# Kernel optimization log

Hardware: AMD Instinct MI355X
Metric: run time of the kernel (lower is better)

## Reference

```python
import jax, jax.numpy as jnp
import numpy as np
import math

B, S, HID = 2, 2048, 2048
NH, NKV, HD = 16, 4, 128
N_REP = NH // NKV
THETA = 1000000.0


def apply_rope(x, position_ids, theta=THETA):
    # x: (B, H, S, D), position_ids: (B, S)
    d = x.shape[-1]
    freqs = 1.0 / (theta ** (jnp.arange(0, d, 2, dtype=jnp.float32) / d))  # (D/2,)
    angles = position_ids.astype(jnp.float32)[:, :, None] * freqs[None, None, :]  # (B,S,D/2)
    cos = jnp.cos(angles)[:, None, :, :]  # (B,1,S,D/2)
    sin = jnp.sin(angles)[:, None, :, :]
    x_even = x[..., 0::2]
    x_odd = x[..., 1::2]
    rot_even = x_even * cos - x_odd * sin
    rot_odd = x_even * sin + x_odd * cos
    out = jnp.stack([rot_even, rot_odd], axis=-1)  # (B,H,S,D/2,2)
    return out.reshape(x.shape)


def setup_inputs() -> dict:
    key = jax.random.key(0)
    ks = jax.random.split(key, 6)
    x = jax.random.normal(ks[0], (B, S, HID), dtype=jnp.float32)
    position_ids = jnp.broadcast_to(jnp.arange(S, dtype=jnp.int64)[None, :], (B, S))
    # causal additive mask: 0 on/below diagonal, large negative above
    causal = jnp.where(jnp.tril(jnp.ones((S, S), dtype=bool)), 0.0, -1e9).astype(jnp.float32)
    attention_mask = jnp.broadcast_to(causal[None, None, :, :], (B, 1, S, S))
    sc = 1.0 / math.sqrt(HID)
    Wq = jax.random.normal(ks[1], (HID, NH * HD), dtype=jnp.float32) * sc
    Wk = jax.random.normal(ks[2], (HID, NKV * HD), dtype=jnp.float32) * sc
    Wv = jax.random.normal(ks[3], (HID, NKV * HD), dtype=jnp.float32) * sc
    Wo = jax.random.normal(ks[4], (NH * HD, HID), dtype=jnp.float32) * sc
    return {"x": x, "position_ids": position_ids, "attention_mask": attention_mask,
            "Wq": Wq, "Wk": Wk, "Wv": Wv, "Wo": Wo}


def reference(x, position_ids, attention_mask, Wq, Wk, Wv, Wo):
    b, s, _ = x.shape
    q = (x @ Wq).reshape(b, s, NH, HD).transpose(0, 2, 1, 3)   # (B,NH,S,D)
    k = (x @ Wk).reshape(b, s, NKV, HD).transpose(0, 2, 1, 3)  # (B,NKV,S,D)
    v = (x @ Wv).reshape(b, s, NKV, HD).transpose(0, 2, 1, 3)
    q = apply_rope(q, position_ids)
    k = apply_rope(k, position_ids)
    # repeat_kv: expand KV heads to match Q heads
    k = jnp.repeat(k, N_REP, axis=1)  # (B,NH,S,D)
    v = jnp.repeat(v, N_REP, axis=1)
    scale = 1.0 / math.sqrt(HD)
    scores = jnp.einsum('bhqd,bhkd->bhqk', q, k) * scale
    scores = scores + attention_mask
    attn = jax.nn.softmax(scores, axis=-1)
    out = jnp.einsum('bhqk,bhkd->bhqd', attn, v)
    out = out.transpose(0, 2, 1, 3).reshape(b, s, NH * HD)
    return out @ Wo
```

## Files before the change

kernel.cpp:

```cpp
#include <hip/hip_runtime.h>
#include <hip/hip_bf16.h>

#define S_LEN 2048
#define HID_D 2048
#define NH 16
#define NKV 4
#define HD 128
#define BATCH 2

typedef __hip_bfloat16 bf16;
using f32x4 = __attribute__((ext_vector_type(4))) float;
using s16x8 = __attribute__((ext_vector_type(8))) short;

struct TrueT { static constexpr bool value = true; };
struct FalseT { static constexpr bool value = false; };

__device__ __forceinline__ f32x4 mfma_16x16x32(s16x8 a, s16x8 b, f32x4 c) {
  return __builtin_amdgcn_mfma_f32_16x16x32_bf16(a, b, c, 0, 0, 0);
}

__device__ __forceinline__ void gload16(const void* g, void* l) {
  __builtin_amdgcn_global_load_lds(
      (const __attribute__((address_space(1))) void*)g,
      (__attribute__((address_space(3))) void*)l, 16, 0, 0);
}

__device__ __forceinline__ unsigned int pk2bf(float a, float b) {
  __hip_bfloat16 lo = __float2bfloat16(a), hi = __float2bfloat16(b);
  return ((unsigned int)*(unsigned short*)&hi << 16) | *(unsigned short*)&lo;
}

__global__ __launch_bounds__(256) void convert_bf16_k(const float* __restrict__ in,
                                                      bf16* __restrict__ out) {
  int i = (blockIdx.x * 256 + threadIdx.x) * 4;
  float4 v = *(const float4*)&in[i];
  out[i + 0] = __float2bfloat16(v.x);
  out[i + 1] = __float2bfloat16(v.y);
  out[i + 2] = __float2bfloat16(v.z);
  out[i + 3] = __float2bfloat16(v.w);
}

__global__ __launch_bounds__(256) void transpose_convert_k(const float* __restrict__ in,
                                                           bf16* __restrict__ out,
                                                           int K, int N) {
  __shared__ float tile[32][33];
  int n0 = blockIdx.x * 32, k0 = blockIdx.y * 32;
  int tx = threadIdx.x, ty = threadIdx.y;
#pragma unroll
  for (int i = ty; i < 32; i += 8) tile[i][tx] = in[(size_t)(k0 + i) * N + n0 + tx];
  __syncthreads();
#pragma unroll
  for (int i = ty; i < 32; i += 8)
    out[(size_t)(n0 + i) * K + k0 + tx] = __float2bfloat16(tile[tx][i]);
}

__global__ __launch_bounds__(512) void gemm256_k(const bf16* __restrict__ A,
                                                 const bf16* __restrict__ Bt,
                                                 float* __restrict__ C,
                                                 int M, int N, int K) {
  __shared__ bf16 Asm[2][256 * 64];
  __shared__ bf16 Bsm[2][256 * 64];
  const int tid = threadIdx.x;
  const int lane = tid & 63, wid = tid >> 6;
  const int fr = lane & 15, hi = lane >> 4;

  const int bid = blockIdx.y * gridDim.x + blockIdx.x;
  const int nwg = gridDim.x * gridDim.y;
  const int swz = (bid & 7) * (nwg >> 3) + (bid >> 3);
  const int m0 = (swz % gridDim.x) * 256;
  const int n0 = (swz / gridDim.x) * 256;

  const bf16* Ag = A + (size_t)m0 * K;
  const bf16* Bg = Bt + (size_t)n0 * K;

  auto stageHalf = [&](const bf16* src, bf16* ldsBase, int hr0, int k0) {
#pragma unroll
    for (int c = 0; c < 2; ++c) {
      int byte = tid * 16 + c * 8192;
      int row = byte >> 7;
      int col = byte & 127;
      int colSw = col ^ ((row & 7) << 4);
      gload16((const char*)(src + (size_t)(hr0 + row) * K + k0) + colSw,
              (char*)ldsBase + hr0 * 128 + byte);
    }
  };

  f32x4 acc[4][4][2];
#pragma unroll
  for (int p = 0; p < 4; ++p)
#pragma unroll
    for (int m = 0; m < 4; ++m)
#pragma unroll
      for (int n = 0; n < 2; ++n) acc[p][m][n] = (f32x4){0.f, 0.f, 0.f, 0.f};

  const int NT = K >> 6;
  stageHalf(Ag, &Asm[0][0], 0, 0);
  stageHalf(Bg, &Bsm[0][0], 0, 0);
  stageHalf(Bg, &Bsm[0][0], 128, 0);
  stageHalf(Ag, &Asm[0][0], 128, 0);
  asm volatile("s_waitcnt vmcnt(4)" ::: "memory");
  __builtin_amdgcn_s_barrier();

  for (int t = 0; t < NT; ++t) {
    const int cur = t & 1;
    const int nxt = cur ^ 1;
    const int kn = (t + 1) << 6;
    const bool more = (t + 1) < NT;
#pragma unroll
    for (int p = 0; p < 4; ++p) {
      const int r0 = (p >> 1) * 128 + (wid >> 2) * 64;
      const int c0 = (p & 1) * 128 + (wid & 3) * 32;
      s16x8 af[2][4], bq[2][2];
#pragma unroll
      for (int ks = 0; ks < 2; ++ks) {
#pragma unroll
        for (int m = 0; m < 4; ++m) {
          int r = r0 + m * 16 + fr;
          int cb = (ks * 64 + hi * 16) ^ ((r & 7) << 4);
          af[ks][m] = *(const s16x8*)((const char*)&Asm[cur][0] + r * 128 + cb);
        }
#pragma unroll
        for (int n = 0; n < 2; ++n) {
          int bn = c0 + n * 16 + fr;
          int cb = (ks * 64 + hi * 16) ^ ((bn & 7) << 4);
          bq[ks][n] = *(const s16x8*)((const char*)&Bsm[cur][0] + bn * 128 + cb);
        }
      }
      if (more) {
        if (p == 0) stageHalf(Ag, &Asm[nxt][0], 0, kn);
        else if (p == 1) stageHalf(Bg, &Bsm[nxt][0], 0, kn);
        else if (p == 2) stageHalf(Bg, &Bsm[nxt][0], 128, kn);
        else stageHalf(Ag, &Asm[nxt][0], 128, kn);
        asm volatile("s_waitcnt vmcnt(4)" ::: "memory");
      } else {
        if (p == 0) asm volatile("s_waitcnt vmcnt(2)" ::: "memory");
        else if (p == 1) asm volatile("s_waitcnt vmcnt(0)" ::: "memory");
      }
      __builtin_amdgcn_s_barrier();

      __builtin_amdgcn_s_setprio(1);
#pragma unroll
      for (int m = 0; m < 4; ++m)
#pragma unroll
        for (int n = 0; n < 2; ++n) {
          acc[p][m][n] = mfma_16x16x32(af[0][m], bq[0][n], acc[p][m][n]);
          acc[p][m][n] = mfma_16x16x32(af[1][m], bq[1][n], acc[p][m][n]);
        }
      __builtin_amdgcn_s_setprio(0);
    }
  }

#pragma unroll
  for (int p = 0; p < 4; ++p) {
    const int r0 = (p >> 1) * 128 + (wid >> 2) * 64;
    const int c0 = (p & 1) * 128 + (wid & 3) * 32;
#pragma unroll
    for (int m = 0; m < 4; ++m)
#pragma unroll
      for (int n = 0; n < 2; ++n) {
        const int row = m0 + r0 + m * 16 + hi * 4;
        const int col = n0 + c0 + n * 16 + fr;
#pragma unroll
        for (int r = 0; r < 4; ++r)
          C[(size_t)(row + r) * N + col] = acc[p][m][n][r];
      }
  }
}

__global__ __launch_bounds__(512) void gemm128n_k(const bf16* __restrict__ A,
                                                  const bf16* __restrict__ Bt,
                                                  float* __restrict__ C,
                                                  int M, int N, int K) {
  __shared__ bf16 Asm[2][256 * 64];
  __shared__ bf16 Bsm[2][128 * 64];
  const int tid = threadIdx.x;
  const int lane = tid & 63, wid = tid >> 6;
  const int fr = lane & 15, hi = lane >> 4;

  const int bid = blockIdx.y * gridDim.x + blockIdx.x;
  const int nwg = gridDim.x * gridDim.y;
  const int swz = (bid & 7) * (nwg >> 3) + (bid >> 3);
  const int m0 = (swz % gridDim.x) * 256;
  const int n0 = (swz / gridDim.x) * 128;

  const bf16* Ag = A + (size_t)m0 * K;
  const bf16* Bg = Bt + (size_t)n0 * K;

  auto stageHalf = [&](const bf16* src, bf16* ldsBase, int hr0, int k0) {
#pragma unroll
    for (int c = 0; c < 2; ++c) {
      int byte = tid * 16 + c * 8192;
      int row = byte >> 7;
      int col = byte & 127;
      int colSw = col ^ ((row & 7) << 4);
      gload16((const char*)(src + (size_t)(hr0 + row) * K + k0) + colSw,
              (char*)ldsBase + hr0 * 128 + byte);
    }
  };

  f32x4 acc[2][4][2];
#pragma unroll
  for (int p = 0; p < 2; ++p)
#pragma unroll
    for (int m = 0; m < 4; ++m)
#pragma unroll
      for (int n = 0; n < 2; ++n) acc[p][m][n] = (f32x4){0.f, 0.f, 0.f, 0.f};

  const int NT = K >> 6;
  stageHalf(Bg, &Bsm[0][0], 0, 0);
  stageHalf(Ag, &Asm[0][0], 0, 0);
  stageHalf(Ag, &Asm[0][0], 128, 0);
  asm volatile("s_waitcnt vmcnt(2)" ::: "memory");
  __builtin_amdgcn_s_barrier();

  for (int t = 0; t < NT; ++t) {
    const int cur = t & 1;
    const int nxt = cur ^ 1;
    const int kn = (t + 1) << 6;
    const bool more = (t + 1) < NT;
#pragma unroll
    for (int p = 0; p < 2; ++p) {
      const int r0 = p * 128 + (wid >> 2) * 64;
      const int c0 = (wid & 3) * 32;
      s16x8 af[2][4], bq[2][2];
#pragma unroll
      for (int ks = 0; ks < 2; ++ks) {
#pragma unroll
        for (int m = 0; m < 4; ++m) {
          int r = r0 + m * 16 + fr;
          int cb = (ks * 64 + hi * 16) ^ ((r & 7) << 4);
          af[ks][m] = *(const s16x8*)((const char*)&Asm[cur][0] + r * 128 + cb);
        }
#pragma unroll
        for (int n = 0; n < 2; ++n) {
          int bn = c0 + n * 16 + fr;
          int cb = (ks * 64 + hi * 16) ^ ((bn & 7) << 4);
          bq[ks][n] = *(const s16x8*)((const char*)&Bsm[cur][0] + bn * 128 + cb);
        }
      }
      if (more) {
        if (p == 0) {
          stageHalf(Bg, &Bsm[nxt][0], 0, kn);
          stageHalf(Ag, &Asm[nxt][0], 0, kn);
        } else {
          stageHalf(Ag, &Asm[nxt][0], 128, kn);
        }
        asm volatile("s_waitcnt vmcnt(2)" ::: "memory");
      } else {
        if (p == 0) asm volatile("s_waitcnt vmcnt(0)" ::: "memory");
      }
      __builtin_amdgcn_s_barrier();

      __builtin_amdgcn_s_setprio(1);
#pragma unroll
      for (int m = 0; m < 4; ++m)
#pragma unroll
        for (int n = 0; n < 2; ++n) {
          acc[p][m][n] = mfma_16x16x32(af[0][m], bq[0][n], acc[p][m][n]);
          acc[p][m][n] = mfma_16x16x32(af[1][m], bq[1][n], acc[p][m][n]);
        }
      __builtin_amdgcn_s_setprio(0);
    }
  }

#pragma unroll
  for (int p = 0; p < 2; ++p) {
    const int r0 = p * 128 + (wid >> 2) * 64;
    const int c0 = (wid & 3) * 32;
#pragma unroll
    for (int m = 0; m < 4; ++m)
#pragma unroll
      for (int n = 0; n < 2; ++n) {
        const int row = m0 + r0 + m * 16 + hi * 4;
        const int col = n0 + c0 + n * 16 + fr;
#pragma unroll
        for (int r = 0; r < 4; ++r)
          C[(size_t)(row + r) * N + col] = acc[p][m][n][r];
      }
  }
}

__global__ __launch_bounds__(256) void rope_q_k(const float* __restrict__ qkv,
                                                const int* __restrict__ pos_ids,
                                                bf16* __restrict__ Q) {
  int idx = blockIdx.x * 256 + threadIdx.x;
  int i = idx & 63;
  int h = (idx >> 6) & 15;
  int s = (idx >> 10) & 2047;
  int b = idx >> 21;
  const float kscale = 0.12751841418861862f;
  float pos = (float)pos_ids[b * S_LEN + s];
  float freq = exp2f((float)i * -0.31143075889569023f);
  float ang = pos * freq;
  float sn, cs;
  sincosf(ang, &sn, &cs);
  const float* src = qkv + (size_t)(b * S_LEN + s) * 3072 + h * HD + 2 * i;
  float e = src[0], o = src[1];
  bf16* dst = Q + ((size_t)(b * NH + h) * S_LEN + s) * HD + 2 * i;
  dst[0] = __float2bfloat16((e * cs - o * sn) * kscale);
  dst[1] = __float2bfloat16((e * sn + o * cs) * kscale);
}

__global__ __launch_bounds__(256) void rope_k_k(const float* __restrict__ qkv,
                                                const int* __restrict__ pos_ids,
                                                bf16* __restrict__ Kd) {
  int idx = blockIdx.x * 256 + threadIdx.x;
  int i = idx & 63;
  int kvh = (idx >> 6) & 3;
  int s = (idx >> 8) & 2047;
  int b = idx >> 19;
  float pos = (float)pos_ids[b * S_LEN + s];
  float freq = exp2f((float)i * -0.31143075889569023f);
  float ang = pos * freq;
  float sn, cs;
  sincosf(ang, &sn, &cs);
  const float* src = qkv + (size_t)(b * S_LEN + s) * 3072 + 2048 + kvh * HD + 2 * i;
  float e = src[0], o = src[1];
  bf16* dst = Kd + ((size_t)(b * NKV + kvh) * S_LEN + s) * HD + 2 * i;
  dst[0] = __float2bfloat16(e * cs - o * sn);
  dst[1] = __float2bfloat16(e * sn + o * cs);
}

__global__ __launch_bounds__(256) void v_trans_k(const float* __restrict__ qkv,
                                                 bf16* __restrict__ Vt) {
  __shared__ float tile[32][33];
  const int tx = threadIdx.x, ty = threadIdx.y;
  const int s0 = blockIdx.x * 32;
  const int d0 = blockIdx.y * 32;
  const int b = blockIdx.z >> 2, kvh = blockIdx.z & 3;
  const float* src = qkv + 2560 + kvh * HD;
#pragma unroll
  for (int i = ty; i < 32; i += 8)
    tile[i][tx] = src[(size_t)(b * S_LEN + s0 + i) * 3072 + d0 + tx];
  __syncthreads();
  bf16* dst = Vt + (size_t)(b * NKV + kvh) * HD * S_LEN;
#pragma unroll
  for (int i = ty; i < 32; i += 8)
    dst[(size_t)(d0 + i) * S_LEN + s0 + tx] = __float2bfloat16(tile[tx][i]);
}

__global__ __launch_bounds__(256) void attn_k(const bf16* __restrict__ Q,
                                              const bf16* __restrict__ K,
                                              const bf16* __restrict__ Vt,
                                              bf16* __restrict__ Aout) {
  __shared__ bf16 Ks[2][64 * 128];
  __shared__ bf16 Vs[2][128 * 64];
  __shared__ bf16 Ps[4][16 * 64];

  const int lane = threadIdx.x & 63;
  const int wid = threadIdx.x >> 6;
  const int fr = lane & 15;
  const int hi = lane >> 4;
  const int pi = blockIdx.x, h = blockIdx.y, b = blockIdx.z;
  const int kvh = h >> 2;
  const bf16* Qh = Q + (size_t)(b * NH + h) * S_LEN * HD;
  const bf16* Kh = K + (size_t)(b * NKV + kvh) * S_LEN * HD;
  const bf16* Vh = Vt + (size_t)(b * NKV + kvh) * HD * S_LEN;

  const int oB = lane * 16;
  const int rinK = oB >> 8;
  const int rinV = oB >> 7;
  bf16* myP = &Ps[wid][0];
  const int pswz = (fr & 7) << 4;

  auto stageKV = [&](int bufi, int kv0) {
#pragma unroll
    for (int c = 0; c < 4; ++c) {
      int absr = wid * 16 + c * 4 + rinK;
      int colb = (oB & 255) ^ (((absr >> 2) & 7) << 4);
      gload16((const char*)Kh + (size_t)(kv0 + absr) * 256 + colb,
              (char*)&Ks[bufi][0] + (wid * 16 + c * 4) * 256);
    }
#pragma unroll
    for (int c = 0; c < 4; ++c) {
      int absd = wid * 32 + c * 8 + rinV;
      int colb = (oB & 127) ^ ((absd & 7) << 4);
      gload16((const char*)Vh + (size_t)absd * (S_LEN * 2) + (size_t)kv0 * 2 + colb,
              (char*)&Vs[bufi][0] + (wid * 32 + c * 8) * 128);
    }
  };

#pragma unroll 1
  for (int t = 0; t < 2; ++t) {
    const int qb = t ? (31 - pi) : pi;
    const int q0w = qb * 64 + wid * 16;
    const int nsteps = qb + 1;

    s16x8 qf[4];
#pragma unroll
    for (int ks = 0; ks < 4; ++ks)
      qf[ks] = *(const s16x8*)&Qh[(size_t)(q0w + fr) * HD + ks * 32 + hi * 8];

    f32x4 o[8];
#pragma unroll
    for (int ds = 0; ds < 8; ++ds) o[ds] = (f32x4){0.f, 0.f, 0.f, 0.f};
    float lacc[4];
#pragma unroll
    for (int r = 0; r < 4; ++r) lacc[r] = 0.f;

    auto doStep = [&](int kv0, int bufc, auto LASTC) {
      constexpr bool LAST = decltype(LASTC)::value;
      f32x4 sg[4];
#pragma unroll
      for (int kv = 0; kv < 4; ++kv) {
        f32x4 a = (f32x4){0.f, 0.f, 0.f, 0.f};
        const int row = 4 * fr + kv;
#pragma unroll
        for (int ks = 0; ks < 4; ++ks) {
          int cb = (ks * 64 + hi * 16) ^ (((row >> 2) & 7) << 4);
          s16x8 kf = *(const s16x8*)((const char*)&Ks[bufc][0] + row * 256 + cb);
          a = mfma_16x16x32(qf[ks], kf, a);
        }
        sg[kv] = a;
      }

#pragma unroll
      for (int r = 0; r < 4; ++r) {
        float p0 = __builtin_exp2f(sg[0][r]);
        float p1 = __builtin_exp2f(sg[1][r]);
        float p2 = __builtin_exp2f(sg[2][r]);
        float p3 = __builtin_exp2f(sg[3][r]);
        if (LAST) {
          const int qrow = q0w + hi * 4 + r;
          const int kb = kv0 + 4 * fr;
          p0 = (kb <= qrow) ? p0 : 0.f;
          p1 = (kb + 1 <= qrow) ? p1 : 0.f;
          p2 = (kb + 2 <= qrow) ? p2 : 0.f;
          p3 = (kb + 3 <= qrow) ? p3 : 0.f;
        }
        lacc[r] += (p0 + p1) + (p2 + p3);
        const int prow = hi * 4 + r;
        uint2 pv;
        pv.x = pk2bf(p0, p1);
        pv.y = pk2bf(p2, p3);
        *(uint2*)((char*)myP + prow * 128 + ((fr * 8) ^ ((prow & 7) << 4))) = pv;
      }
      __builtin_amdgcn_wave_barrier();

      s16x8 pf[2];
#pragma unroll
      for (int g = 0; g < 2; ++g) {
        int cb = (g * 64 + hi * 16) ^ pswz;
        pf[g] = *(const s16x8*)((const char*)myP + fr * 128 + cb);
      }
      __builtin_amdgcn_wave_barrier();
#pragma unroll
      for (int ds = 0; ds < 8; ++ds) {
#pragma unroll
        for (int g = 0; g < 2; ++g) {
          int d = ds * 16 + fr;
          int cb = (g * 64 + hi * 16) ^ ((d & 7) << 4);
          s16x8 vf = *(const s16x8*)((const char*)&Vs[bufc][0] + d * 128 + cb);
          o[ds] = mfma_16x16x32(pf[g], vf, o[ds]);
        }
      }
    };

    int buf = 0;
    stageKV(0, 0);
    __syncthreads();

    for (int s = 0; s < nsteps - 1; ++s) {
      stageKV(buf ^ 1, s * 64 + 64);
      doStep(s * 64, buf, FalseT{});
      __syncthreads();
      buf ^= 1;
    }
    doStep((nsteps - 1) * 64, buf, TrueT{});
    __syncthreads();

#pragma unroll
    for (int r = 0; r < 4; ++r) {
      float l = lacc[r];
      l += __shfl_xor(l, 1, 16);
      l += __shfl_xor(l, 2, 16);
      l += __shfl_xor(l, 4, 16);
      l += __shfl_xor(l, 8, 16);
      float inv = 1.0f / l;
      const int srow = q0w + hi * 4 + r;
      bf16* orow = Aout + ((size_t)b * S_LEN + srow) * HID_D + h * HD;
#pragma unroll
      for (int ds = 0; ds < 8; ++ds)
        orow[ds * 16 + fr] = __float2bfloat16(o[ds][r] * inv);
    }
  }
}

extern "C" void kernel_launch(void* const* d_in, const int* in_sizes, int n_in,
                              void* d_out, int out_size, void* d_ws, size_t ws_size,
                              hipStream_t stream) {
  const float* x = (const float*)d_in[0];
  const int* pos = (const int*)d_in[1];
  const float* Wq = (const float*)d_in[3];
  const float* Wk = (const float*)d_in[4];
  const float* Wv = (const float*)d_in[5];
  const float* Wo = (const float*)d_in[6];
  float* out = (float*)d_out;

  char* ws = (char*)d_ws;
  size_t off = 0;
  auto alloc = [&](size_t bytes) {
    char* p = ws + off;
    off += (bytes + 255) & ~(size_t)255;
    return p;
  };
  bf16* xb = (bf16*)alloc((size_t)4096 * 2048 * 2);
  bf16* WqkvT = (bf16*)alloc((size_t)3072 * 2048 * 2);
  bf16* WoT = (bf16*)alloc((size_t)2048 * 2048 * 2);
  float* qkv = (float*)alloc((size_t)4096 * 3072 * 4);
  bf16* Qb = (bf16*)alloc((size_t)BATCH * NH * S_LEN * HD * 2);
  bf16* Kb = (bf16*)alloc((size_t)BATCH * NKV * S_LEN * HD * 2);
  bf16* Vtb = (bf16*)alloc((size_t)BATCH * NKV * HD * S_LEN * 2);
  bf16* aout = (bf16*)qkv;

  convert_bf16_k<<<8192, 256, 0, stream>>>(x, xb);
  dim3 tb(32, 8);
  transpose_convert_k<<<dim3(64, 64), tb, 0, stream>>>(Wq, WqkvT, 2048, 2048);
  transpose_convert_k<<<dim3(16, 64), tb, 0, stream>>>(Wk, WqkvT + (size_t)2048 * 2048, 2048, 512);
  transpose_convert_k<<<dim3(16, 64), tb, 0, stream>>>(Wv, WqkvT + (size_t)2560 * 2048, 2048, 512);
  transpose_convert_k<<<dim3(64, 64), tb, 0, stream>>>(Wo, WoT, 2048, 2048);

  gemm256_k<<<dim3(16, 12), 512, 0, stream>>>(xb, WqkvT, qkv, 4096, 3072, 2048);

  rope_q_k<<<16384, 256, 0, stream>>>(qkv, pos, Qb);
  rope_k_k<<<4096, 256, 0, stream>>>(qkv, pos, Kb);
  v_trans_k<<<dim3(64, 4, 8), tb, 0, stream>>>(qkv, Vtb);

  attn_k<<<dim3(16, NH, BATCH), 256, 0, stream>>>(Qb, Kb, Vtb, aout);

  gemm128n_k<<<dim3(16, 16), 512, 0, stream>>>(aout, WoT, out, 4096, 2048, 2048);
}
```

Baseline: 218.4 us.

## Store QKV projection in bf16 and widen attention query tile to 128 rows

The QKV GEMM now writes bf16 instead of fp32. This halves the intermediate buffer traffic read by the rope and V-transpose kernels. The attention kernel now handles 32 query rows per wave (128 per block) with two accumulator sets, so each K/V fragment loaded from LDS feeds two MFMAs. The grid is halved, which doubles per-wave register use and reduces the number of blocks available for load balancing. The qkv intermediate also loses precision by being rounded to bf16 before the rope step.

```diff
diff --git a/kernel.cpp b/kernel.cpp
--- a/kernel.cpp
+++ b/kernel.cpp
@@ -11,9 +11,6 @@
 typedef __hip_bfloat16 bf16;
 using f32x4 = __attribute__((ext_vector_type(4))) float;
 using s16x8 = __attribute__((ext_vector_type(8))) short;
-
-struct TrueT { static constexpr bool value = true; };
-struct FalseT { static constexpr bool value = false; };
 
 __device__ __forceinline__ f32x4 mfma_16x16x32(s16x8 a, s16x8 b, f32x4 c) {
   return __builtin_amdgcn_mfma_f32_16x16x32_bf16(a, b, c, 0, 0, 0);
@@ -56,7 +53,7 @@
 
 __global__ __launch_bounds__(512) void gemm256_k(const bf16* __restrict__ A,
                                                  const bf16* __restrict__ Bt,
-                                                 float* __restrict__ C,
+                                                 bf16* __restrict__ C,
                                                  int M, int N, int K) {
   __shared__ bf16 Asm[2][256 * 64];
   __shared__ bf16 Bsm[2][256 * 64];
@@ -162,7 +159,7 @@
         const int col = n0 + c0 + n * 16 + fr;
 #pragma unroll
         for (int r = 0; r < 4; ++r)
-          C[(size_t)(row + r) * N + col] = acc[p][m][n][r];
+          C[(size_t)(row + r) * N + col] = __float2bfloat16(acc[p][m][n][r]);
       }
   }
 }
@@ -280,7 +277,7 @@
   }
 }
 
-__global__ __launch_bounds__(256) void rope_q_k(const float* __restrict__ qkv,
+__global__ __launch_bounds__(256) void rope_q_k(const bf16* __restrict__ qkv,
                                                 const int* __restrict__ pos_ids,
                                                 bf16* __restrict__ Q) {
   int idx = blockIdx.x * 256 + threadIdx.x;
@@ -294,14 +291,14 @@
   float ang = pos * freq;
   float sn, cs;
   sincosf(ang, &sn, &cs);
-  const float* src = qkv + (size_t)(b * S_LEN + s) * 3072 + h * HD + 2 * i;
-  float e = src[0], o = src[1];
+  const bf16* src = qkv + (size_t)(b * S_LEN + s) * 3072 + h * HD + 2 * i;
+  float e = __bfloat162float(src[0]), o = __bfloat162float(src[1]);
   bf16* dst = Q + ((size_t)(b * NH + h) * S_LEN + s) * HD + 2 * i;
   dst[0] = __float2bfloat16((e * cs - o * sn) * kscale);
   dst[1] = __float2bfloat16((e * sn + o * cs) * kscale);
 }
 
-__global__ __launch_bounds__(256) void rope_k_k(const float* __restrict__ qkv,
+__global__ __launch_bounds__(256) void rope_k_k(const bf16* __restrict__ qkv,
                                                 const int* __restrict__ pos_ids,
                                                 bf16* __restrict__ Kd) {
   int idx = blockIdx.x * 256 + threadIdx.x;
@@ -314,29 +311,29 @@
   float ang = pos * freq;
   float sn, cs;
   sincosf(ang, &sn, &cs);
-  const float* src = qkv + (size_t)(b * S_LEN + s) * 3072 + 2048 + kvh * HD + 2 * i;
-  float e = src[0], o = src[1];
+  const bf16* src = qkv + (size_t)(b * S_LEN + s) * 3072 + 2048 + kvh * HD + 2 * i;
+  float e = __bfloat162float(src[0]), o = __bfloat162float(src[1]);
   bf16* dst = Kd + ((size_t)(b * NKV + kvh) * S_LEN + s) * HD + 2 * i;
   dst[0] = __float2bfloat16(e * cs - o * sn);
   dst[1] = __float2bfloat16(e * sn + o * cs);
 }
 
-__global__ __launch_bounds__(256) void v_trans_k(const float* __restrict__ qkv,
+__global__ __launch_bounds__(256) void v_trans_k(const bf16* __restrict__ qkv,
                                                  bf16* __restrict__ Vt) {
-  __shared__ float tile[32][33];
+  __shared__ unsigned short tile[32][33];
   const int tx = threadIdx.x, ty = threadIdx.y;
   const int s0 = blockIdx.x * 32;
   const int d0 = blockIdx.y * 32;
   const int b = blockIdx.z >> 2, kvh = blockIdx.z & 3;
-  const float* src = qkv + 2560 + kvh * HD;
+  const unsigned short* src = (const unsigned short*)qkv + 2560 + kvh * HD;
 #pragma unroll
   for (int i = ty; i < 32; i += 8)
     tile[i][tx] = src[(size_t)(b * S_LEN + s0 + i) * 3072 + d0 + tx];
   __syncthreads();
-  bf16* dst = Vt + (size_t)(b * NKV + kvh) * HD * S_LEN;
+  unsigned short* dst = (unsigned short*)Vt + (size_t)(b * NKV + kvh) * HD * S_LEN;
 #pragma unroll
   for (int i = ty; i < 32; i += 8)
-    dst[(size_t)(d0 + i) * S_LEN + s0 + tx] = __float2bfloat16(tile[tx][i]);
+    dst[(size_t)(d0 + i) * S_LEN + s0 + tx] = tile[tx][i];
 }
 
 __global__ __launch_bounds__(256) void attn_k(const bf16* __restrict__ Q,
@@ -345,7 +342,7 @@
                                               bf16* __restrict__ Aout) {
   __shared__ bf16 Ks[2][64 * 128];
   __shared__ bf16 Vs[2][128 * 64];
-  __shared__ bf16 Ps[4][16 * 64];
+  __shared__ bf16 Ps[4][32 * 64];
 
   const int lane = threadIdx.x & 63;
   const int wid = threadIdx.x >> 6;
@@ -382,107 +379,123 @@
 
 #pragma unroll 1
   for (int t = 0; t < 2; ++t) {
-    const int qb = t ? (31 - pi) : pi;
-    const int q0w = qb * 64 + wid * 16;
-    const int nsteps = qb + 1;
-
-    s16x8 qf[4];
-#pragma unroll
-    for (int ks = 0; ks < 4; ++ks)
-      qf[ks] = *(const s16x8*)&Qh[(size_t)(q0w + fr) * HD + ks * 32 + hi * 8];
-
-    f32x4 o[8];
-#pragma unroll
-    for (int ds = 0; ds < 8; ++ds) o[ds] = (f32x4){0.f, 0.f, 0.f, 0.f};
-    float lacc[4];
-#pragma unroll
-    for (int r = 0; r < 4; ++r) lacc[r] = 0.f;
-
-    auto doStep = [&](int kv0, int bufc, auto LASTC) {
-      constexpr bool LAST = decltype(LASTC)::value;
-      f32x4 sg[4];
-#pragma unroll
-      for (int kv = 0; kv < 4; ++kv) {
-        f32x4 a = (f32x4){0.f, 0.f, 0.f, 0.f};
-        const int row = 4 * fr + kv;
-#pragma unroll
-        for (int ks = 0; ks < 4; ++ks) {
-          int cb = (ks * 64 + hi * 16) ^ (((row >> 2) & 7) << 4);
-          s16x8 kf = *(const s16x8*)((const char*)&Ks[bufc][0] + row * 256 + cb);
-          a = mfma_16x16x32(qf[ks], kf, a);
-        }
-        sg[kv] = a;
-      }
-
-#pragma unroll
-      for (int r = 0; r < 4; ++r) {
-        float p0 = __builtin_exp2f(sg[0][r]);
-        float p1 = __builtin_exp2f(sg[1][r]);
-        float p2 = __builtin_exp2f(sg[2][r]);
-        float p3 = __builtin_exp2f(sg[3][r]);
-        if (LAST) {
-          const int qrow = q0w + hi * 4 + r;
-          const int kb = kv0 + 4 * fr;
-          p0 = (kb <= qrow) ? p0 : 0.f;
-          p1 = (kb + 1 <= qrow) ? p1 : 0.f;
-          p2 = (kb + 2 <= qrow) ? p2 : 0.f;
-          p3 = (kb + 3 <= qrow) ? p3 : 0.f;
-        }
-        lacc[r] += (p0 + p1) + (p2 + p3);
-        const int prow = hi * 4 + r;
-        uint2 pv;
-        pv.x = pk2bf(p0, p1);
-        pv.y = pk2bf(p2, p3);
-        *(uint2*)((char*)myP + prow * 128 + ((fr * 8) ^ ((prow & 7) << 4))) = pv;
-      }
-      __builtin_amdgcn_wave_barrier();
-
-      s16x8 pf[2];
-#pragma unroll
-      for (int g = 0; g < 2; ++g) {
-        int cb = (g * 64 + hi * 16) ^ pswz;
-        pf[g] = *(const s16x8*)((const char*)myP + fr * 128 + cb);
-      }
-      __builtin_amdgcn_wave_barrier();
-#pragma unroll
-      for (int ds = 0; ds < 8; ++ds) {
-#pragma unroll
-        for (int g = 0; g < 2; ++g) {
-          int d = ds * 16 + fr;
-          int cb = (g * 64 + hi * 16) ^ ((d & 7) << 4);
-          s16x8 vf = *(const s16x8*)((const char*)&Vs[bufc][0] + d * 128 + cb);
-          o[ds] = mfma_16x16x32(pf[g], vf, o[ds]);
-        }
-      }
-    };
+    const int qb = t ? (15 - pi) : pi;
+    const int q0w = qb * 128 + wid * 32;
+    const int nsteps = 2 * qb + 2;
+
+    s16x8 qf[2][4];
+#pragma unroll
+    for (int u = 0; u < 2; ++u)
+#pragma unroll
+      for (int ks = 0; ks < 4; ++ks)
+        qf[u][ks] = *(const s16x8*)&Qh[(size_t)(q0w + u * 16 + fr) * HD + ks * 32 + hi * 8];
+
+    f32x4 o[2][8];
+#pragma unroll
+    for (int u = 0; u < 2; ++u)
+#pragma unroll
+      for (int ds = 0; ds < 8; ++ds) o[u][ds] = (f32x4){0.f, 0.f, 0.f, 0.f};
+    float lacc[2][4];
+#pragma unroll
+    for (int u = 0; u < 2; ++u)
+#pragma unroll
+      for (int r = 0; r < 4; ++r) lacc[u][r] = 0.f;
 
     int buf = 0;
     stageKV(0, 0);
     __syncthreads();
 
-    for (int s = 0; s < nsteps - 1; ++s) {
-      stageKV(buf ^ 1, s * 64 + 64);
-      doStep(s * 64, buf, FalseT{});
+    for (int s = 0; s < nsteps; ++s) {
+      const int kv0 = s * 64;
+      if (s + 1 < nsteps) stageKV(buf ^ 1, kv0 + 64);
+
+      if (kv0 <= q0w + 31) {
+        const bool diag = (kv0 >> 6) == (q0w >> 6);
+        f32x4 sg[2][4];
+#pragma unroll
+        for (int u = 0; u < 2; ++u)
+#pragma unroll
+          for (int kv = 0; kv < 4; ++kv) sg[u][kv] = (f32x4){0.f, 0.f, 0.f, 0.f};
+#pragma unroll
+        for (int kv = 0; kv < 4; ++kv) {
+          const int row = 4 * fr + kv;
+#pragma unroll
+          for (int ks = 0; ks < 4; ++ks) {
+            int cb = (ks * 64 + hi * 16) ^ (((row >> 2) & 7) << 4);
+            s16x8 kf = *(const s16x8*)((const char*)&Ks[buf][0] + row * 256 + cb);
+            sg[0][kv] = mfma_16x16x32(qf[0][ks], kf, sg[0][kv]);
+            sg[1][kv] = mfma_16x16x32(qf[1][ks], kf, sg[1][kv]);
+          }
+        }
+
+#pragma unroll
+        for (int u = 0; u < 2; ++u)
+#pragma unroll
+          for (int r = 0; r < 4; ++r) {
+            float p0 = __builtin_exp2f(sg[u][0][r]);
+            float p1 = __builtin_exp2f(sg[u][1][r]);
+            float p2 = __builtin_exp2f(sg[u][2][r]);
+            float p3 = __builtin_exp2f(sg[u][3][r]);
+            if (diag) {
+              const int qrow = q0w + u * 16 + hi * 4 + r;
+              const int kb = kv0 + 4 * fr;
+              p0 = (kb <= qrow) ? p0 : 0.f;
+              p1 = (kb + 1 <= qrow) ? p1 : 0.f;
+              p2 = (kb + 2 <= qrow) ? p2 : 0.f;
+              p3 = (kb + 3 <= qrow) ? p3 : 0.f;
+            }
+            lacc[u][r] += (p0 + p1) + (p2 + p3);
+            const int prow = u * 16 + hi * 4 + r;
+            uint2 pv;
+            pv.x = pk2bf(p0, p1);
+            pv.y = pk2bf(p2, p3);
+            *(uint2*)((char*)myP + prow * 128 + ((fr * 8) ^ ((prow & 7) << 4))) = pv;
+          }
+        __builtin_amdgcn_wave_barrier();
+
+        s16x8 pf[2][2];
+#pragma unroll
+        for (int u = 0; u < 2; ++u)
+#pragma unroll
+          for (int g = 0; g < 2; ++g) {
+            int prow = u * 16 + fr;
+            int cb = (g * 64 + hi * 16) ^ pswz;
+            pf[u][g] = *(const s16x8*)((const char*)myP + prow * 128 + cb);
+          }
+        __builtin_amdgcn_wave_barrier();
+#pragma unroll
+        for (int ds = 0; ds < 8; ++ds) {
+#pragma unroll
+          for (int g = 0; g < 2; ++g) {
+            int d = ds * 16 + fr;
+            int cb = (g * 64 + hi * 16) ^ ((d & 7) << 4);
+            s16x8 vf = *(const s16x8*)((const char*)&Vs[buf][0] + d * 128 + cb);
+            o[0][ds] = mfma_16x16x32(pf[0][g], vf, o[0][ds]);
+            o[1][ds] = mfma_16x16x32(pf[1][g], vf, o[1][ds]);
+          }
+        }
+      }
+
       __syncthreads();
       buf ^= 1;
     }
-    doStep((nsteps - 1) * 64, buf, TrueT{});
-    __syncthreads();
-
-#pragma unroll
-    for (int r = 0; r < 4; ++r) {
-      float l = lacc[r];
-      l += __shfl_xor(l, 1, 16);
-      l += __shfl_xor(l, 2, 16);
-      l += __shfl_xor(l, 4, 16);
-      l += __shfl_xor(l, 8, 16);
-      float inv = 1.0f / l;
-      const int srow = q0w + hi * 4 + r;
-      bf16* orow = Aout + ((size_t)b * S_LEN + srow) * HID_D + h * HD;
-#pragma unroll
-      for (int ds = 0; ds < 8; ++ds)
-        orow[ds * 16 + fr] = __float2bfloat16(o[ds][r] * inv);
-    }
+
+#pragma unroll
+    for (int u = 0; u < 2; ++u)
+#pragma unroll
+      for (int r = 0; r < 4; ++r) {
+        float l = lacc[u][r];
+        l += __shfl_xor(l, 1, 16);
+        l += __shfl_xor(l, 2, 16);
+        l += __shfl_xor(l, 4, 16);
+        l += __shfl_xor(l, 8, 16);
+        float inv = 1.0f / l;
+        const int srow = q0w + u * 16 + hi * 4 + r;
+        bf16* orow = Aout + ((size_t)b * S_LEN + srow) * HID_D + h * HD;
+#pragma unroll
+        for (int ds = 0; ds < 8; ++ds)
+          orow[ds * 16 + fr] = __float2bfloat16(o[u][ds][r] * inv);
+      }
   }
 }
 
@@ -507,7 +520,7 @@
   bf16* xb = (bf16*)alloc((size_t)4096 * 2048 * 2);
   bf16* WqkvT = (bf16*)alloc((size_t)3072 * 2048 * 2);
   bf16* WoT = (bf16*)alloc((size_t)2048 * 2048 * 2);
-  float* qkv = (float*)alloc((size_t)4096 * 3072 * 4);
+  bf16* qkv = (bf16*)alloc((size_t)4096 * 3072 * 2);
   bf16* Qb = (bf16*)alloc((size_t)BATCH * NH * S_LEN * HD * 2);
   bf16* Kb = (bf16*)alloc((size_t)BATCH * NKV * S_LEN * HD * 2);
   bf16* Vtb = (bf16*)alloc((size_t)BATCH * NKV * HD * S_LEN * 2);
@@ -526,7 +539,7 @@
   rope_k_k<<<4096, 256, 0, stream>>>(qkv, pos, Kb);
   v_trans_k<<<dim3(64, 4, 8), tb, 0, stream>>>(qkv, Vtb);
 
-  attn_k<<<dim3(16, NH, BATCH), 256, 0, stream>>>(Qb, Kb, Vtb, aout);
+  attn_k<<<dim3(8, NH, BATCH), 256, 0, stream>>>(Qb, Kb, Vtb, aout);
 
   gemm128n_k<<<dim3(16, 16), 512, 0, stream>>>(aout, WoT, out, 4096, 2048, 2048);
 }
```

Measured after the change: 243.1 us. +11.3%, slower.

## Store QKV projection in bf16 and retile output GEMM to 128x128 blocks

Applied to the files above, without the earlier changes.

The QKV GEMM now writes bf16 instead of fp32, which halves the intermediate buffer traffic. The rope and V-transpose kernels are changed to read bf16, and the V transpose becomes a plain 16-bit copy. Separately, the output projection GEMM is replaced by a 128x128-tile, 256-thread kernel launched on 512 blocks instead of 256, which gives more blocks across the CUs. The new kernel waits on all loads (vmcnt(0)) each iteration, so there is less load/compute overlap, and rounding q/k/v to bf16 before rope adds a small precision loss.

```diff
diff --git a/kernel.cpp b/kernel.cpp
--- a/kernel.cpp
+++ b/kernel.cpp
@@ -56,7 +56,7 @@
 
 __global__ __launch_bounds__(512) void gemm256_k(const bf16* __restrict__ A,
                                                  const bf16* __restrict__ Bt,
-                                                 float* __restrict__ C,
+                                                 bf16* __restrict__ C,
                                                  int M, int N, int K) {
   __shared__ bf16 Asm[2][256 * 64];
   __shared__ bf16 Bsm[2][256 * 64];
@@ -162,16 +162,16 @@
         const int col = n0 + c0 + n * 16 + fr;
 #pragma unroll
         for (int r = 0; r < 4; ++r)
-          C[(size_t)(row + r) * N + col] = acc[p][m][n][r];
+          C[(size_t)(row + r) * N + col] = __float2bfloat16(acc[p][m][n][r]);
       }
   }
 }
 
-__global__ __launch_bounds__(512) void gemm128n_k(const bf16* __restrict__ A,
-                                                  const bf16* __restrict__ Bt,
-                                                  float* __restrict__ C,
-                                                  int M, int N, int K) {
-  __shared__ bf16 Asm[2][256 * 64];
+__global__ __launch_bounds__(256) void gemm128sq_k(const bf16* __restrict__ A,
+                                                   const bf16* __restrict__ Bt,
+                                                   float* __restrict__ C,
+                                                   int M, int N, int K) {
+  __shared__ bf16 Asm[2][128 * 64];
   __shared__ bf16 Bsm[2][128 * 64];
   const int tid = threadIdx.x;
   const int lane = tid & 63, wid = tid >> 6;
@@ -180,37 +180,37 @@
   const int bid = blockIdx.y * gridDim.x + blockIdx.x;
   const int nwg = gridDim.x * gridDim.y;
   const int swz = (bid & 7) * (nwg >> 3) + (bid >> 3);
-  const int m0 = (swz % gridDim.x) * 256;
+  const int m0 = (swz % gridDim.x) * 128;
   const int n0 = (swz / gridDim.x) * 128;
 
   const bf16* Ag = A + (size_t)m0 * K;
   const bf16* Bg = Bt + (size_t)n0 * K;
 
-  auto stageHalf = [&](const bf16* src, bf16* ldsBase, int hr0, int k0) {
-#pragma unroll
-    for (int c = 0; c < 2; ++c) {
-      int byte = tid * 16 + c * 8192;
+  auto stageT = [&](const bf16* src, bf16* ldsBase, int k0) {
+#pragma unroll
+    for (int c = 0; c < 4; ++c) {
+      int byte = tid * 16 + c * 4096;
       int row = byte >> 7;
       int col = byte & 127;
       int colSw = col ^ ((row & 7) << 4);
-      gload16((const char*)(src + (size_t)(hr0 + row) * K + k0) + colSw,
-              (char*)ldsBase + hr0 * 128 + byte);
+      gload16((const char*)(src + (size_t)row * K + k0) + colSw,
+              (char*)ldsBase + byte);
     }
   };
 
-  f32x4 acc[2][4][2];
-#pragma unroll
-  for (int p = 0; p < 2; ++p)
-#pragma unroll
-    for (int m = 0; m < 4; ++m)
-#pragma unroll
-      for (int n = 0; n < 2; ++n) acc[p][m][n] = (f32x4){0.f, 0.f, 0.f, 0.f};
-
+  f32x4 acc[4][4];
+#pragma unroll
+  for (int m = 0; m < 4; ++m)
+#pragma unroll
+    for (int n = 0; n < 4; ++n) acc[m][n] = (f32x4){0.f, 0.f, 0.f, 0.f};
+
+  const int r0 = (wid >> 1) * 64;
+  const int c0 = (wid & 1) * 64;
   const int NT = K >> 6;
-  stageHalf(Bg, &Bsm[0][0], 0, 0);
-  stageHalf(Ag, &Asm[0][0], 0, 0);
-  stageHalf(Ag, &Asm[0][0], 128, 0);
-  asm volatile("s_waitcnt vmcnt(2)" ::: "memory");
+
+  stageT(Ag, &Asm[0][0], 0);
+  stageT(Bg, &Bsm[0][0], 0);
+  asm volatile("s_waitcnt vmcnt(0)" ::: "memory");
   __builtin_amdgcn_s_barrier();
 
   for (int t = 0; t < NT; ++t) {
@@ -220,34 +220,26 @@
     const bool more = (t + 1) < NT;
 #pragma unroll
     for (int p = 0; p < 2; ++p) {
-      const int r0 = p * 128 + (wid >> 2) * 64;
-      const int c0 = (wid & 3) * 32;
-      s16x8 af[2][4], bq[2][2];
-#pragma unroll
-      for (int ks = 0; ks < 2; ++ks) {
-#pragma unroll
-        for (int m = 0; m < 4; ++m) {
-          int r = r0 + m * 16 + fr;
-          int cb = (ks * 64 + hi * 16) ^ ((r & 7) << 4);
-          af[ks][m] = *(const s16x8*)((const char*)&Asm[cur][0] + r * 128 + cb);
-        }
-#pragma unroll
-        for (int n = 0; n < 2; ++n) {
-          int bn = c0 + n * 16 + fr;
-          int cb = (ks * 64 + hi * 16) ^ ((bn & 7) << 4);
-          bq[ks][n] = *(const s16x8*)((const char*)&Bsm[cur][0] + bn * 128 + cb);
-        }
-      }
-      if (more) {
-        if (p == 0) {
-          stageHalf(Bg, &Bsm[nxt][0], 0, kn);
-          stageHalf(Ag, &Asm[nxt][0], 0, kn);
-        } else {
-          stageHalf(Ag, &Asm[nxt][0], 128, kn);
-        }
-        asm volatile("s_waitcnt vmcnt(2)" ::: "memory");
+      s16x8 af[4], bq[4];
+#pragma unroll
+      for (int m = 0; m < 4; ++m) {
+        int r = r0 + m * 16 + fr;
+        int cb = (p * 64 + hi * 16) ^ ((r & 7) << 4);
+        af[m] = *(const s16x8*)((const char*)&Asm[cur][0] + r * 128 + cb);
+      }
+#pragma unroll
+      for (int n = 0; n < 4; ++n) {
+        int bn = c0 + n * 16 + fr;
+        int cb = (p * 64 + hi * 16) ^ ((bn & 7) << 4);
+        bq[n] = *(const s16x8*)((const char*)&Bsm[cur][0] + bn * 128 + cb);
+      }
+      if (p == 0) {
+        if (more) {
+          stageT(Ag, &Asm[nxt][0], kn);
+          stageT(Bg, &Bsm[nxt][0], kn);
+        }
       } else {
-        if (p == 0) asm volatile("s_waitcnt vmcnt(0)" ::: "memory");
+        asm volatile("s_waitcnt vmcnt(0)" ::: "memory");
       }
       __builtin_amdgcn_s_barrier();
 
@@ -255,32 +247,25 @@
 #pragma unroll
       for (int m = 0; m < 4; ++m)
 #pragma unroll
-        for (int n = 0; n < 2; ++n) {
-          acc[p][m][n] = mfma_16x16x32(af[0][m], bq[0][n], acc[p][m][n]);
-          acc[p][m][n] = mfma_16x16x32(af[1][m], bq[1][n], acc[p][m][n]);
-        }
+        for (int n = 0; n < 4; ++n)
+          acc[m][n] = mfma_16x16x32(af[m], bq[n], acc[m][n]);
       __builtin_amdgcn_s_setprio(0);
     }
   }
 
 #pragma unroll
-  for (int p = 0; p < 2; ++p) {
-    const int r0 = p * 128 + (wid >> 2) * 64;
-    const int c0 = (wid & 3) * 32;
-#pragma unroll
-    for (int m = 0; m < 4; ++m)
-#pragma unroll
-      for (int n = 0; n < 2; ++n) {
-        const int row = m0 + r0 + m * 16 + hi * 4;
-        const int col = n0 + c0 + n * 16 + fr;
-#pragma unroll
-        for (int r = 0; r < 4; ++r)
-          C[(size_t)(row + r) * N + col] = acc[p][m][n][r];
-      }
-  }
-}
-
-__global__ __launch_bounds__(256) void rope_q_k(const float* __restrict__ qkv,
+  for (int m = 0; m < 4; ++m)
+#pragma unroll
+    for (int n = 0; n < 4; ++n) {
+      const int row = m0 + r0 + m * 16 + hi * 4;
+      const int col = n0 + c0 + n * 16 + fr;
+#pragma unroll
+      for (int r = 0; r < 4; ++r)
+        C[(size_t)(row + r) * N + col] = acc[m][n][r];
+    }
+}
+
+__global__ __launch_bounds__(256) void rope_q_k(const bf16* __restrict__ qkv,
                                                 const int* __restrict__ pos_ids,
                                                 bf16* __restrict__ Q) {
   int idx = blockIdx.x * 256 + threadIdx.x;
@@ -294,14 +279,14 @@
   float ang = pos * freq;
   float sn, cs;
   sincosf(ang, &sn, &cs);
-  const float* src = qkv + (size_t)(b * S_LEN + s) * 3072 + h * HD + 2 * i;
-  float e = src[0], o = src[1];
+  const bf16* src = qkv + (size_t)(b * S_LEN + s) * 3072 + h * HD + 2 * i;
+  float e = __bfloat162float(src[0]), o = __bfloat162float(src[1]);
   bf16* dst = Q + ((size_t)(b * NH + h) * S_LEN + s) * HD + 2 * i;
   dst[0] = __float2bfloat16((e * cs - o * sn) * kscale);
   dst[1] = __float2bfloat16((e * sn + o * cs) * kscale);
 }
 
-__global__ __launch_bounds__(256) void rope_k_k(const float* __restrict__ qkv,
+__global__ __launch_bounds__(256) void rope_k_k(const bf16* __restrict__ qkv,
                                                 const int* __restrict__ pos_ids,
                                                 bf16* __restrict__ Kd) {
   int idx = blockIdx.x * 256 + threadIdx.x;
@@ -314,29 +299,29 @@
   float ang = pos * freq;
   float sn, cs;
   sincosf(ang, &sn, &cs);
-  const float* src = qkv + (size_t)(b * S_LEN + s) * 3072 + 2048 + kvh * HD + 2 * i;
-  float e = src[0], o = src[1];
+  const bf16* src = qkv + (size_t)(b * S_LEN + s) * 3072 + 2048 + kvh * HD + 2 * i;
+  float e = __bfloat162float(src[0]), o = __bfloat162float(src[1]);
   bf16* dst = Kd + ((size_t)(b * NKV + kvh) * S_LEN + s) * HD + 2 * i;
   dst[0] = __float2bfloat16(e * cs - o * sn);
   dst[1] = __float2bfloat16(e * sn + o * cs);
 }
 
-__global__ __launch_bounds__(256) void v_trans_k(const float* __restrict__ qkv,
+__global__ __launch_bounds__(256) void v_trans_k(const bf16* __restrict__ qkv,
                                                  bf16* __restrict__ Vt) {
-  __shared__ float tile[32][33];
+  __shared__ unsigned short tile[32][33];
   const int tx = threadIdx.x, ty = threadIdx.y;
   const int s0 = blockIdx.x * 32;
   const int d0 = blockIdx.y * 32;
   const int b = blockIdx.z >> 2, kvh = blockIdx.z & 3;
-  const float* src = qkv + 2560 + kvh * HD;
+  const unsigned short* src = (const unsigned short*)qkv + 2560 + kvh * HD;
 #pragma unroll
   for (int i = ty; i < 32; i += 8)
     tile[i][tx] = src[(size_t)(b * S_LEN + s0 + i) * 3072 + d0 + tx];
   __syncthreads();
-  bf16* dst = Vt + (size_t)(b * NKV + kvh) * HD * S_LEN;
+  unsigned short* dst = (unsigned short*)Vt + (size_t)(b * NKV + kvh) * HD * S_LEN;
 #pragma unroll
   for (int i = ty; i < 32; i += 8)
-    dst[(size_t)(d0 + i) * S_LEN + s0 + tx] = __float2bfloat16(tile[tx][i]);
+    dst[(size_t)(d0 + i) * S_LEN + s0 + tx] = tile[tx][i];
 }
 
 __global__ __launch_bounds__(256) void attn_k(const bf16* __restrict__ Q,
@@ -507,7 +492,7 @@
   bf16* xb = (bf16*)alloc((size_t)4096 * 2048 * 2);
   bf16* WqkvT = (bf16*)alloc((size_t)3072 * 2048 * 2);
   bf16* WoT = (bf16*)alloc((size_t)2048 * 2048 * 2);
-  float* qkv = (float*)alloc((size_t)4096 * 3072 * 4);
+  bf16* qkv = (bf16*)alloc((size_t)4096 * 3072 * 2);
   bf16* Qb = (bf16*)alloc((size_t)BATCH * NH * S_LEN * HD * 2);
   bf16* Kb = (bf16*)alloc((size_t)BATCH * NKV * S_LEN * HD * 2);
   bf16* Vtb = (bf16*)alloc((size_t)BATCH * NKV * HD * S_LEN * 2);
@@ -528,5 +513,5 @@
 
   attn_k<<<dim3(16, NH, BATCH), 256, 0, stream>>>(Qb, Kb, Vtb, aout);
 
-  gemm128n_k<<<dim3(16, 16), 512, 0, stream>>>(aout, WoT, out, 4096, 2048, 2048);
-}
+  gemm128sq_k<<<dim3(32, 16), 256, 0, stream>>>(aout, WoT, out, 4096, 2048, 2048);
+}
```

Result: faster. 207.3 us (-5.1%).
